# Performance work log

Hardware: AMD Instinct MI355X
Metric: run time of the kernel (lower is better)

Reference implementation:

```python
import jax, jax.numpy as jnp
import numpy as np

BS, SLEN, EM = 32, 4096, 256


def setup_inputs() -> dict:
    key = jax.random.key(0)
    ks = jax.random.split(key, 8)
    word_embedded = jax.random.normal(ks[0], (BS, SLEN, EM), dtype=jnp.float32)
    # valid-token mask: first `length` tokens valid per row (True = keep)
    lengths = jax.random.randint(ks[1], (BS, 1), SLEN // 2, SLEN + 1)
    mask = jnp.arange(SLEN)[None, :] < lengths  # (BS, SLEN) bool
    s = 1.0 / np.sqrt(EM)
    w_query = jax.random.uniform(ks[2], (EM, 1), minval=-1.0, maxval=1.0, dtype=jnp.float32)  # Linear(1, em, bias=False)
    wq = jax.random.uniform(ks[3], (EM, EM), minval=-s, maxval=s, dtype=jnp.float32)
    bq = jax.random.uniform(ks[4], (EM,), minval=-s, maxval=s, dtype=jnp.float32)
    wk = jax.random.uniform(ks[5], (EM, EM), minval=-s, maxval=s, dtype=jnp.float32)
    bk = jax.random.uniform(ks[6], (EM,), minval=-s, maxval=s, dtype=jnp.float32)
    se = 1.0 / np.sqrt(2 * EM)
    we = jax.random.uniform(ks[7], (1, 2 * EM), minval=-se, maxval=se, dtype=jnp.float32)
    be = jnp.zeros((1,), dtype=jnp.float32)
    return {"word_embedded": word_embedded, "mask": mask, "w_query": w_query,
            "wq": wq, "bq": bq, "wk": wk, "bk": bk, "we": we, "be": be}


def reference(word_embedded, mask, w_query, wq, bq, wk, bk, we, be):
    bs, slen, em = word_embedded.shape
    # query = Linear(1, em, no bias) applied to ones -> each row is w_query[:, 0]
    q = jnp.broadcast_to(w_query[:, 0], (bs, em))          # (bs, em)
    qp = jax.nn.relu(q @ wq.T + bq)                        # (bs, em); dropout is identity at eval
    k = jax.nn.relu(word_embedded @ wk.T + bk)             # (bs, slen, em)
    # proj_e(tanh(cat(q, k))) == tanh(q)@we_q + tanh(k)@we_k + be (tanh is elementwise),
    # so we avoid materializing the (bs, slen, 2*em) concat.
    we_q, we_k = we[0, :em], we[0, em:]
    energy = jnp.tanh(qp) @ we_q                           # (bs,)
    energy = energy[:, None] + jnp.tanh(k) @ we_k + be[0]  # (bs, slen)
    # torch: energy.masked_fill_(~mask, 1e-45)
    energy = jnp.where(mask, energy, jnp.float32(1e-45))
    attn_weights = jax.nn.softmax(energy, axis=1)          # (bs, slen)
    sent_embedded = jnp.einsum('bs,bse->be', attn_weights, word_embedded)  # (bs, em)
    return sent_embedded
```

## Files before the change

### kernel.cpp

```cpp
#include <hip/hip_runtime.h>

#define BS   32
#define SLEN 4096
#define EM   256
#define NROWS (BS * SLEN)

typedef __attribute__((ext_vector_type(8))) short bf16x8;
typedef __attribute__((ext_vector_type(4))) float f32x4;

#define WS_WKB   0
#define WS_EN    32768
#define WS_CONST 294912
#define WS_W     294928
#define WS_PART  426000

__device__ inline short f2bf(float x) {
  union { float f; unsigned u; } v; v.f = x;
  unsigned r = v.u + 0x7fffu + ((v.u >> 16) & 1u);
  return (short)(r >> 16);
}

__device__ inline unsigned cvtpk(float lo, float hi) {
  unsigned r;
  asm("v_cvt_pk_bf16_f32 %0, %1, %2" : "=v"(r) : "v"(lo), "v"(hi));
  return r;
}
__device__ inline bf16x8 cvt8(float4 a, float4 b) {
  union { bf16x8 v; unsigned u[4]; } r;
  r.u[0] = cvtpk(a.x, a.y);
  r.u[1] = cvtpk(a.z, a.w);
  r.u[2] = cvtpk(b.x, b.y);
  r.u[3] = cvtpk(b.z, b.w);
  return r.v;
}

#define GLOAD_LDS16(g, l)                                                  \
  __builtin_amdgcn_global_load_lds(                                        \
      (const __attribute__((address_space(1))) unsigned int*)(g),          \
      (__attribute__((address_space(3))) unsigned int*)(l), 16, 0, 0)

__global__ __launch_bounds__(256) void k0_cvt(const float* __restrict__ wk,
                                              unsigned short* __restrict__ wkb2) {
  int gid = blockIdx.x * 256 + threadIdx.x;
  int e = gid >> 5, kq = gid & 31;
  const float* src = wk + (size_t)e * EM + kq * 8;
  float4 v0 = *(const float4*)src;
  float4 v1 = *(const float4*)(src + 4);
  bf16x8 pk;
  pk[0] = f2bf(v0.x); pk[1] = f2bf(v0.y); pk[2] = f2bf(v0.z); pk[3] = f2bf(v0.w);
  pk[4] = f2bf(v1.x); pk[5] = f2bf(v1.y); pk[6] = f2bf(v1.z); pk[7] = f2bf(v1.w);
  *(bf16x8*)(wkb2 + ((size_t)kq * 256 + e) * 8) = pk;
}

__global__ __launch_bounds__(256) void k0b_qscalar(const float* __restrict__ w_query,
                                                   const float* __restrict__ wq,
                                                   const float* __restrict__ bq,
                                                   const float* __restrict__ we,
                                                   const float* __restrict__ be,
                                                   float* __restrict__ outc) {
  int t = threadIdx.x;
  const float* row = wq + (size_t)t * EM;
  float4 a4 = make_float4(0.f, 0.f, 0.f, 0.f);
#pragma unroll 8
  for (int j = 0; j < 64; ++j) {
    float4 r = *(const float4*)(row + j * 4);
    float4 q = *(const float4*)(w_query + j * 4);
    a4.x = fmaf(r.x, q.x, a4.x);
    a4.y = fmaf(r.y, q.y, a4.y);
    a4.z = fmaf(r.z, q.z, a4.z);
    a4.w = fmaf(r.w, q.w, a4.w);
  }
  float a = (a4.x + a4.y) + (a4.z + a4.w) + bq[t];
  float kv = fmaxf(a, 0.f);
  float z = __expf(kv + kv);
  float v = we[t] * (1.f - __fdividef(2.f, z + 1.f));
#pragma unroll
  for (int off = 32; off >= 1; off >>= 1) v += __shfl_xor(v, off, 64);
  __shared__ float red[4];
  if ((t & 63) == 0) red[t >> 6] = v;
  __syncthreads();
  if (t == 0) outc[0] = red[0] + red[1] + red[2] + red[3] + be[0];
}

__global__ __launch_bounds__(512) void k1_energy(const float* __restrict__ X,
                                                 const unsigned short* __restrict__ wkb2,
                                                 const float* __restrict__ bk,
                                                 const float* __restrict__ we,
                                                 float* __restrict__ energy) {
  __shared__ char Bs[65536];
  const int tid = threadIdx.x;
  const int l = tid & 63;
  const int w = tid >> 6;
  const int lr = l & 15, lk = l >> 4;
  const int ch = blockIdx.x & 1;
  const int blk = blockIdx.x >> 1;
  const int row0 = blk * 256 + w * 32;

#pragma unroll
  for (int q = 0; q < 8; ++q) {
    int g = w * 8 + q;
    int kq = g >> 1;
    const char* src = (const char*)wkb2 + kq * 4096 + ch * 2048 + (g & 1) * 1024 + l * 16;
    GLOAD_LDS16(src, Bs + g * 1024);
  }

  f32x4 acc[2][8];
#pragma unroll
  for (int n = 0; n < 8; ++n) {
    float b = bk[ch * 128 + n * 16 + lr];
    acc[0][n] = (f32x4){b, b, b, b};
    acc[1][n] = acc[0][n];
  }

  const float* xbase = X + (size_t)(row0 + lr) * EM + lk * 8;
  float4 c00 = *(const float4*)(xbase);
  float4 c01 = *(const float4*)(xbase + 4);
  float4 c10 = *(const float4*)(xbase + 16 * EM);
  float4 c11 = *(const float4*)(xbase + 16 * EM + 4);

  __syncthreads();

#pragma unroll
  for (int s = 0; s < 8; ++s) {
    float4 n00, n01, n10, n11;
    if (s < 7) {
      const float* nx = xbase + (s + 1) * 32;
      n00 = *(const float4*)(nx);
      n01 = *(const float4*)(nx + 4);
      n10 = *(const float4*)(nx + 16 * EM);
      n11 = *(const float4*)(nx + 16 * EM + 4);
    }
    bf16x8 a0 = cvt8(c00, c01);
    bf16x8 a1 = cvt8(c10, c11);
    const char* bp = Bs + s * 8192 + lk * 2048 + lr * 16;
#pragma unroll
    for (int n = 0; n < 8; ++n) {
      bf16x8 bfr = *(const bf16x8*)(bp + n * 256);
      acc[0][n] = __builtin_amdgcn_mfma_f32_16x16x32_bf16(a0, bfr, acc[0][n], 0, 0, 0);
      acc[1][n] = __builtin_amdgcn_mfma_f32_16x16x32_bf16(a1, bfr, acc[1][n], 0, 0, 0);
    }
    c00 = n00; c01 = n01; c10 = n10; c11 = n11;
  }

  float sumw = 0.f, w2[8];
#pragma unroll
  for (int n = 0; n < 8; ++n) {
    float wv = we[EM + ch * 128 + n * 16 + lr];
    sumw += wv;
    w2[n] = -2.f * wv;
  }
  float* eout = energy + (size_t)ch * NROWS;
#pragma unroll
  for (int i = 0; i < 2; ++i) {
#pragma unroll
    for (int r = 0; r < 4; ++r) {
      float p = sumw;
#pragma unroll
      for (int n = 0; n < 8; ++n) {
        float kv = fmaxf(acc[i][n][r], 0.f);
        float z = __expf(kv + kv);
        p = fmaf(w2[n], __fdividef(1.f, z + 1.f), p);
      }
#pragma unroll
      for (int off = 1; off <= 8; off <<= 1) p += __shfl_xor(p, off, 16);
      if (lr == 0) eout[row0 + i * 16 + lk * 4 + r] = p;
    }
  }
}

__global__ __launch_bounds__(256) void k2_softmax(const float* __restrict__ energy,
                                                  const unsigned char* __restrict__ mask,
                                                  const float* __restrict__ cptr,
                                                  float* __restrict__ wout) {
  const int b = blockIdx.x;
  const int t = threadIdx.x;
  const float C = cptr[0];
  const bool mask_is_byte = (mask[1] | mask[2] | mask[3]) != 0;
  const int* mask32 = (const int*)mask;
  const float* eb0 = energy + (size_t)b * SLEN;
  const float* eb1 = energy + NROWS + (size_t)b * SLEN;
  float v[16];
  float m = -3.4e38f;
#pragma unroll
  for (int i = 0; i < 16; ++i) {
    int s = t + i * 256;
    int mv = mask_is_byte ? (int)mask[(size_t)b * SLEN + s]
                          : mask32[(size_t)b * SLEN + s];
    float x = mv ? (eb0[s] + eb1[s] + C) : 1.4012984643248171e-45f;
    v[i] = x;
    m = fmaxf(m, x);
  }
  __shared__ float red[8];
#pragma unroll
  for (int off = 32; off >= 1; off >>= 1) m = fmaxf(m, __shfl_xor(m, off, 64));
  if ((t & 63) == 0) red[t >> 6] = m;
  __syncthreads();
  m = fmaxf(fmaxf(red[0], red[1]), fmaxf(red[2], red[3]));
  float s_ = 0.f;
#pragma unroll
  for (int i = 0; i < 16; ++i) {
    v[i] = __expf(v[i] - m);
    s_ += v[i];
  }
#pragma unroll
  for (int off = 32; off >= 1; off >>= 1) s_ += __shfl_xor(s_, off, 64);
  if ((t & 63) == 0) red[4 + (t >> 6)] = s_;
  __syncthreads();
  float inv = 1.f / (red[4] + red[5] + red[6] + red[7]);
  float* wb = wout + (size_t)b * SLEN;
#pragma unroll
  for (int i = 0; i < 16; ++i) wb[t + i * 256] = v[i] * inv;
}

__global__ __launch_bounds__(256) void k3_wsum(const float* __restrict__ X,
                                               const float* __restrict__ w,
                                               float* __restrict__ part) {
  __shared__ float red[4][EM];
  const int b = blockIdx.x >> 6;
  const int ch = blockIdx.x & 63;
  const int g = threadIdx.x >> 6;
  const int l = threadIdx.x & 63;
  const int s0 = ch * 64 + g * 16;
  const float* xb = X + (size_t)b * SLEN * EM;
  const float* wb = w + (size_t)b * SLEN;
  float4 acc = make_float4(0.f, 0.f, 0.f, 0.f);
#pragma unroll
  for (int i = 0; i < 16; ++i) {
    int s = s0 + i;
    float ws_ = wb[s];
    float4 v = *(const float4*)(xb + (size_t)s * EM + l * 4);
    acc.x = fmaf(ws_, v.x, acc.x);
    acc.y = fmaf(ws_, v.y, acc.y);
    acc.z = fmaf(ws_, v.z, acc.z);
    acc.w = fmaf(ws_, v.w, acc.w);
  }
  *(float4*)(&red[g][l * 4]) = acc;
  __syncthreads();
  if (g == 0) {
    float4 r0 = *(const float4*)(&red[0][l * 4]);
    float4 r1 = *(const float4*)(&red[1][l * 4]);
    float4 r2 = *(const float4*)(&red[2][l * 4]);
    float4 r3 = *(const float4*)(&red[3][l * 4]);
    float4 o;
    o.x = (r0.x + r1.x) + (r2.x + r3.x);
    o.y = (r0.y + r1.y) + (r2.y + r3.y);
    o.z = (r0.z + r1.z) + (r2.z + r3.z);
    o.w = (r0.w + r1.w) + (r2.w + r3.w);
    *(float4*)(part + (size_t)blockIdx.x * EM + l * 4) = o;
  }
}

__global__ __launch_bounds__(256) void k4_reduce(const float* __restrict__ part,
                                                 float* __restrict__ out) {
  const int b = blockIdx.x;
  const int e = threadIdx.x;
  float s = 0.f;
#pragma unroll 8
  for (int k = 0; k < 64; ++k) s += part[((size_t)b * 64 + k) * EM + e];
  out[(size_t)b * EM + e] = s;
}

extern "C" void kernel_launch(void* const* d_in, const int* in_sizes, int n_in,
                              void* d_out, int out_size, void* d_ws, size_t ws_size,
                              hipStream_t stream) {
  const float* X = (const float*)d_in[0];
  const unsigned char* mask = (const unsigned char*)d_in[1];
  const float* w_query = (const float*)d_in[2];
  const float* wq = (const float*)d_in[3];
  const float* bq = (const float*)d_in[4];
  const float* wk = (const float*)d_in[5];
  const float* bk = (const float*)d_in[6];
  const float* we = (const float*)d_in[7];
  const float* be = (const float*)d_in[8];
  float* out = (float*)d_out;
  float* ws = (float*)d_ws;

  unsigned short* wkb2 = (unsigned short*)(ws + WS_WKB);
  float* energy = ws + WS_EN;
  float* cscalar = ws + WS_CONST;
  float* weights = ws + WS_W;
  float* part = ws + WS_PART;

  k0_cvt<<<32, 256, 0, stream>>>(wk, wkb2);
  k0b_qscalar<<<1, 256, 0, stream>>>(w_query, wq, bq, we, be, cscalar);
  k1_energy<<<1024, 512, 0, stream>>>(X, wkb2, bk, we, energy);
  k2_softmax<<<BS, 256, 0, stream>>>(energy, mask, cscalar, weights);
  k3_wsum<<<BS * 64, 256, 0, stream>>>(X, weights, part);
  k4_reduce<<<BS, 256, 0, stream>>>(part, out);
}
```

Baseline: 280.5 us.

## Split energy GEMM into four column chunks with smaller blocks and deeper prefetch

```diff
diff --git a/kernel.cpp b/kernel.cpp
--- a/kernel.cpp
+++ b/kernel.cpp
@@ -10,9 +10,8 @@
 
 #define WS_WKB   0
 #define WS_EN    32768
-#define WS_CONST 294912
-#define WS_W     294928
-#define WS_PART  426000
+#define WS_CONST 557056
+#define WS_W     557072
 
 __device__ inline short f2bf(float x) {
   union { float f; unsigned u; } v; v.f = x;
@@ -82,70 +81,74 @@
   if (t == 0) outc[0] = red[0] + red[1] + red[2] + red[3] + be[0];
 }
 
-__global__ __launch_bounds__(512) void k1_energy(const float* __restrict__ X,
+__global__ __launch_bounds__(256) void k1_energy(const float* __restrict__ X,
                                                  const unsigned short* __restrict__ wkb2,
                                                  const float* __restrict__ bk,
                                                  const float* __restrict__ we,
                                                  float* __restrict__ energy) {
-  __shared__ char Bs[65536];
+  __shared__ char Bs[32768];
   const int tid = threadIdx.x;
   const int l = tid & 63;
   const int w = tid >> 6;
   const int lr = l & 15, lk = l >> 4;
-  const int ch = blockIdx.x & 1;
-  const int blk = blockIdx.x >> 1;
-  const int row0 = blk * 256 + w * 32;
+  const int ch = blockIdx.x >> 10;
+  const int blk = blockIdx.x & 1023;
+  const int row0 = blk * 128 + w * 32;
 
 #pragma unroll
   for (int q = 0; q < 8; ++q) {
-    int g = w * 8 + q;
-    int kq = g >> 1;
-    const char* src = (const char*)wkb2 + kq * 4096 + ch * 2048 + (g & 1) * 1024 + l * 16;
-    GLOAD_LDS16(src, Bs + g * 1024);
-  }
-
-  f32x4 acc[2][8];
-#pragma unroll
-  for (int n = 0; n < 8; ++n) {
-    float b = bk[ch * 128 + n * 16 + lr];
+    int kq = w * 8 + q;
+    const char* src = (const char*)wkb2 + kq * 4096 + ch * 1024 + l * 16;
+    GLOAD_LDS16(src, Bs + kq * 1024);
+  }
+
+  f32x4 acc[2][4];
+#pragma unroll
+  for (int n = 0; n < 4; ++n) {
+    float b = bk[ch * 64 + n * 16 + lr];
     acc[0][n] = (f32x4){b, b, b, b};
     acc[1][n] = acc[0][n];
   }
 
   const float* xbase = X + (size_t)(row0 + lr) * EM + lk * 8;
-  float4 c00 = *(const float4*)(xbase);
-  float4 c01 = *(const float4*)(xbase + 4);
-  float4 c10 = *(const float4*)(xbase + 16 * EM);
-  float4 c11 = *(const float4*)(xbase + 16 * EM + 4);
+  float4 pf[3][4];
+#pragma unroll
+  for (int p = 0; p < 2; ++p) {
+    const float* nx = xbase + p * 32;
+    pf[p][0] = *(const float4*)(nx);
+    pf[p][1] = *(const float4*)(nx + 4);
+    pf[p][2] = *(const float4*)(nx + 16 * EM);
+    pf[p][3] = *(const float4*)(nx + 16 * EM + 4);
+  }
 
   __syncthreads();
 
 #pragma unroll
   for (int s = 0; s < 8; ++s) {
-    float4 n00, n01, n10, n11;
-    if (s < 7) {
-      const float* nx = xbase + (s + 1) * 32;
-      n00 = *(const float4*)(nx);
-      n01 = *(const float4*)(nx + 4);
-      n10 = *(const float4*)(nx + 16 * EM);
-      n11 = *(const float4*)(nx + 16 * EM + 4);
+    if (s < 6) {
+      const int d = (s + 2) % 3;
+      const float* nx = xbase + (s + 2) * 32;
+      pf[d][0] = *(const float4*)(nx);
+      pf[d][1] = *(const float4*)(nx + 4);
+      pf[d][2] = *(const float4*)(nx + 16 * EM);
+      pf[d][3] = *(const float4*)(nx + 16 * EM + 4);
     }
-    bf16x8 a0 = cvt8(c00, c01);
-    bf16x8 a1 = cvt8(c10, c11);
-    const char* bp = Bs + s * 8192 + lk * 2048 + lr * 16;
-#pragma unroll
-    for (int n = 0; n < 8; ++n) {
+    const int c = s % 3;
+    bf16x8 a0 = cvt8(pf[c][0], pf[c][1]);
+    bf16x8 a1 = cvt8(pf[c][2], pf[c][3]);
+    const char* bp = Bs + (s * 4 + lk) * 1024 + lr * 16;
+#pragma unroll
+    for (int n = 0; n < 4; ++n) {
       bf16x8 bfr = *(const bf16x8*)(bp + n * 256);
       acc[0][n] = __builtin_amdgcn_mfma_f32_16x16x32_bf16(a0, bfr, acc[0][n], 0, 0, 0);
       acc[1][n] = __builtin_amdgcn_mfma_f32_16x16x32_bf16(a1, bfr, acc[1][n], 0, 0, 0);
     }
-    c00 = n00; c01 = n01; c10 = n10; c11 = n11;
-  }
-
-  float sumw = 0.f, w2[8];
-#pragma unroll
-  for (int n = 0; n < 8; ++n) {
-    float wv = we[EM + ch * 128 + n * 16 + lr];
+  }
+
+  float sumw = 0.f, w2[4];
+#pragma unroll
+  for (int n = 0; n < 4; ++n) {
+    float wv = we[EM + ch * 64 + n * 16 + lr];
     sumw += wv;
     w2[n] = -2.f * wv;
   }
@@ -156,7 +159,7 @@
     for (int r = 0; r < 4; ++r) {
       float p = sumw;
 #pragma unroll
-      for (int n = 0; n < 8; ++n) {
+      for (int n = 0; n < 4; ++n) {
         float kv = fmaxf(acc[i][n][r], 0.f);
         float z = __expf(kv + kv);
         p = fmaf(w2[n], __fdividef(1.f, z + 1.f), p);
@@ -178,7 +181,9 @@
   const bool mask_is_byte = (mask[1] | mask[2] | mask[3]) != 0;
   const int* mask32 = (const int*)mask;
   const float* eb0 = energy + (size_t)b * SLEN;
-  const float* eb1 = energy + NROWS + (size_t)b * SLEN;
+  const float* eb1 = eb0 + NROWS;
+  const float* eb2 = eb1 + NROWS;
+  const float* eb3 = eb2 + NROWS;
   float v[16];
   float m = -3.4e38f;
 #pragma unroll
@@ -186,7 +191,8 @@
     int s = t + i * 256;
     int mv = mask_is_byte ? (int)mask[(size_t)b * SLEN + s]
                           : mask32[(size_t)b * SLEN + s];
-    float x = mv ? (eb0[s] + eb1[s] + C) : 1.4012984643248171e-45f;
+    float x = mv ? ((eb0[s] + eb1[s]) + (eb2[s] + eb3[s]) + C)
+                 : 1.4012984643248171e-45f;
     v[i] = x;
     m = fmaxf(m, x);
   }
@@ -279,11 +285,11 @@
   float* energy = ws + WS_EN;
   float* cscalar = ws + WS_CONST;
   float* weights = ws + WS_W;
-  float* part = ws + WS_PART;
+  float* part = ws + WS_EN;
 
   k0_cvt<<<32, 256, 0, stream>>>(wk, wkb2);
   k0b_qscalar<<<1, 256, 0, stream>>>(w_query, wq, bq, we, be, cscalar);
-  k1_energy<<<1024, 512, 0, stream>>>(X, wkb2, bk, we, energy);
+  k1_energy<<<4096, 256, 0, stream>>>(X, wkb2, bk, we, energy);
   k2_softmax<<<BS, 256, 0, stream>>>(energy, mask, cscalar, weights);
   k3_wsum<<<BS * 64, 256, 0, stream>>>(X, weights, part);
   k4_reduce<<<BS, 256, 0, stream>>>(part, out);
```

New measurement: 312.8 us. 1.11x slower.
